# Optimization experiments

Measured on AMD Instinct MI355X. Metric: run time of the kernel, lower is better.

Reference implementation:

```python
import jax, jax.numpy as jnp
import numpy as np

DIM = 192
RC = 16
M = 64
LN_EPS = 1e-5
NORM_EPS = 1e-12


def _layernorm(x, g, b):
    mu = jnp.mean(x, axis=-1, keepdims=True)
    var = jnp.mean((x - mu) ** 2, axis=-1, keepdims=True)
    return (x - mu) / jnp.sqrt(var + LN_EPS) * g + b


def _l2norm(x):
    n = jnp.sqrt(jnp.sum(x * x, axis=-1, keepdims=True))
    return x / jnp.maximum(n, NORM_EPS)


def setup_inputs() -> dict:
    key = jax.random.key(0)
    ks = jax.random.split(key, 12)
    B, N = 8, 16384
    s_q = 1.0 / np.sqrt(DIM)
    inp = {
        "x": jax.random.normal(ks[0], (B, N, DIM), jnp.float32),
        "dict_tokens": jax.random.normal(ks[1], (B, M, DIM), jnp.float32),
        "H": 128,
        "W": 128,
        "wq_w": jax.random.normal(ks[2], (DIM, RC), jnp.float32) * s_q,
        "wq_b": jnp.zeros((RC,), jnp.float32),
        "wk_w": jax.random.normal(ks[3], (DIM, RC), jnp.float32) * s_q,
        "wk_b": jnp.zeros((RC,), jnp.float32),
        "wv_w": jax.random.normal(ks[4], (DIM, DIM), jnp.float32) * s_q,
        "wv_b": jnp.zeros((DIM,), jnp.float32),
        "qn_g": jnp.ones((RC,), jnp.float32),
        "qn_b": jnp.zeros((RC,), jnp.float32),
        "kn_g": jnp.ones((RC,), jnp.float32),
        "kn_b": jnp.zeros((RC,), jnp.float32),
        "conv_w": jax.random.normal(ks[5], (DIM, 1, 3, 3), jnp.float32) / 3.0,
        "conv_b": jnp.zeros((DIM,), jnp.float32),
        "temperature": jnp.ones((1,), jnp.float32),
    }
    return inp


def reference(x, dict_tokens, H, W, wq_w, wq_b, wk_w, wk_b, wv_w, wv_b,
              qn_g, qn_b, kn_g, kn_b, conv_w, conv_b, temperature):
    # q: (B,N,rc), k: (B,M,rc)
    q = _l2norm(_layernorm(x @ wq_w + wq_b, qn_g, qn_b))
    k = _l2norm(_layernorm(dict_tokens @ wk_w + wk_b, kn_g, kn_b))
    # cosine-similarity attention with clamped temperature
    attn = jnp.einsum("bnr,bmr->bnm", q, k) / jnp.maximum(temperature, 0.5)
    attn = jax.nn.softmax(attn, axis=-1)
    # value + depthwise-conv refinement over the M token axis (Mx1 image)
    v = dict_tokens @ wv_w + wv_b                       # (B,M,C)
    v_img = jnp.transpose(v, (0, 2, 1))[..., None]      # (B,C,M,1)
    v_img = jax.lax.conv_general_dilated(
        v_img, conv_w, window_strides=(1, 1), padding=((1, 1), (1, 1)),
        dimension_numbers=("NCHW", "OIHW", "NCHW"), feature_group_count=DIM)
    v_img = v_img + conv_b[None, :, None, None]
    v_img = jax.nn.gelu(v_img, approximate=False)
    v = jnp.transpose(v_img[..., 0], (0, 2, 1))         # (B,M,C)
    out = jnp.einsum("bnm,bmc->bnc", attn, v)           # (B,N,C)
    return out, attn
```

## Files before the change

### kernel.cpp

```cpp
#include <hip/hip_runtime.h>
#include <math.h>

#define B_   8
#define N_   16384
#define M_   64
#define C_   192
#define RC_  16

__global__ __launch_bounds__(256) void k_v_kernel(
    const float* __restrict__ dict, const float* __restrict__ wv_w,
    const float* __restrict__ wv_b, float* __restrict__ ws_v)
{
    const int idx = blockIdx.x * 256 + threadIdx.x;
    const int c   = idx % C_;
    const int row = idx / C_;
    const float* dr = dict + row * C_;
    float acc = wv_b[c];
    #pragma unroll 4
    for (int d = 0; d < C_; ++d)
        acc = fmaf(dr[d], wv_w[d * C_ + c], acc);
    ws_v[idx] = acc;
}

__global__ __launch_bounds__(256) void k_k_kernel(
    const float* __restrict__ dict, const float* __restrict__ wk_w,
    const float* __restrict__ wk_b, const float* __restrict__ kn_g,
    const float* __restrict__ kn_b, float* __restrict__ ws_k)
{
    const int b  = blockIdx.x;
    const int m  = threadIdx.x >> 2;
    const int j4 = threadIdx.x & 3;
    const int c0 = j4 * 4;
    const float* dr = dict + (b * M_ + m) * C_;

    float a0 = wk_b[c0+0], a1 = wk_b[c0+1], a2 = wk_b[c0+2], a3 = wk_b[c0+3];
    #pragma unroll 4
    for (int d4 = 0; d4 < C_/4; ++d4) {
        const float4 xv = ((const float4*)dr)[d4];
        const float4 w0 = *(const float4*)&wk_w[(d4*4+0)*RC_ + c0];
        const float4 w1 = *(const float4*)&wk_w[(d4*4+1)*RC_ + c0];
        const float4 w2 = *(const float4*)&wk_w[(d4*4+2)*RC_ + c0];
        const float4 w3 = *(const float4*)&wk_w[(d4*4+3)*RC_ + c0];
        a0 = fmaf(xv.x, w0.x, a0); a1 = fmaf(xv.x, w0.y, a1); a2 = fmaf(xv.x, w0.z, a2); a3 = fmaf(xv.x, w0.w, a3);
        a0 = fmaf(xv.y, w1.x, a0); a1 = fmaf(xv.y, w1.y, a1); a2 = fmaf(xv.y, w1.z, a2); a3 = fmaf(xv.y, w1.w, a3);
        a0 = fmaf(xv.z, w2.x, a0); a1 = fmaf(xv.z, w2.y, a1); a2 = fmaf(xv.z, w2.z, a2); a3 = fmaf(xv.z, w2.w, a3);
        a0 = fmaf(xv.w, w3.x, a0); a1 = fmaf(xv.w, w3.y, a1); a2 = fmaf(xv.w, w3.z, a2); a3 = fmaf(xv.w, w3.w, a3);
    }
    float s  = a0 + a1 + a2 + a3;
    float ss = a0*a0 + a1*a1 + a2*a2 + a3*a3;
    s  += __shfl_xor(s, 1);  s  += __shfl_xor(s, 2);
    ss += __shfl_xor(ss, 1); ss += __shfl_xor(ss, 2);
    const float mu   = s * (1.0f/16.0f);
    const float var  = ss * (1.0f/16.0f) - mu*mu;
    const float rstd = rsqrtf(var + 1e-5f);
    const float4 g4 = *(const float4*)&kn_g[c0];
    const float4 b4 = *(const float4*)&kn_b[c0];
    float y0 = (a0 - mu) * rstd * g4.x + b4.x;
    float y1 = (a1 - mu) * rstd * g4.y + b4.y;
    float y2 = (a2 - mu) * rstd * g4.z + b4.z;
    float y3 = (a3 - mu) * rstd * g4.w + b4.w;
    float n2 = y0*y0 + y1*y1 + y2*y2 + y3*y3;
    n2 += __shfl_xor(n2, 1); n2 += __shfl_xor(n2, 2);
    const float inv = 1.0f / fmaxf(sqrtf(n2), 1e-12f);
    float4 o; o.x = y0*inv; o.y = y1*inv; o.z = y2*inv; o.w = y3*inv;
    *(float4*)&ws_k[(b * M_ + m) * RC_ + c0] = o;
}

__global__ __launch_bounds__(256) void k_conv_kernel(
    const float* __restrict__ ws_v, const float* __restrict__ conv_w,
    const float* __restrict__ conv_b, float* __restrict__ ws_vg)
{
    const int idx = blockIdx.x * 256 + threadIdx.x;
    const int c   = idx % C_;
    const int m   = (idx / C_) % M_;
    const float ctr = ws_v[idx];
    const float up  = (m > 0)      ? ws_v[idx - C_] : 0.0f;
    const float dn  = (m < M_ - 1) ? ws_v[idx + C_] : 0.0f;
    const float w0 = conv_w[c*9 + 1];
    const float w1 = conv_w[c*9 + 4];
    const float w2 = conv_w[c*9 + 7];
    float t = conv_b[c];
    t = fmaf(up, w0, t); t = fmaf(ctr, w1, t); t = fmaf(dn, w2, t);
    ws_vg[idx] = 0.5f * t * (1.0f + erff(t * 0.70710678118654752f));
}

__global__ __launch_bounds__(256, 2) void k_main_kernel(
    const float* __restrict__ x, const float* __restrict__ ws_k,
    const float* __restrict__ ws_vg,
    const float* __restrict__ wq_w, const float* __restrict__ wq_b,
    const float* __restrict__ qn_g, const float* __restrict__ qn_b,
    const float* __restrict__ temp,
    float* __restrict__ out, float* __restrict__ attn_out)
{
    __shared__ float vg_s[M_ * C_];
    __shared__ float attn_s[M_ * 68];
    __shared__ float q_s[M_ * 20];
    __shared__ float k_s[M_ * RC_];

    const int tid = threadIdx.x;
    const int b   = blockIdx.x >> 8;
    const int n0  = (blockIdx.x & 255) * M_;

    {
        const float4* src = (const float4*)(ws_vg + b * (M_ * C_));
        float4*       dst = (float4*)vg_s;
        #pragma unroll
        for (int i = 0; i < 12; ++i)
            dst[tid + 256 * i] = src[tid + 256 * i];
        ((float4*)k_s)[tid] = ((const float4*)(ws_k + b * (M_ * RC_)))[tid];
    }

    const int r  = tid >> 2;
    const int j4 = tid & 3;
    const int c0 = j4 * 4;

    const float* xr = x + (size_t)(b * N_ + n0 + r) * C_;
    float a0 = wq_b[c0+0], a1 = wq_b[c0+1], a2 = wq_b[c0+2], a3 = wq_b[c0+3];
    #pragma unroll 4
    for (int d4 = 0; d4 < C_/4; ++d4) {
        const float4 xv = ((const float4*)xr)[d4];
        const float4 w0 = *(const float4*)&wq_w[(d4*4+0)*RC_ + c0];
        const float4 w1 = *(const float4*)&wq_w[(d4*4+1)*RC_ + c0];
        const float4 w2 = *(const float4*)&wq_w[(d4*4+2)*RC_ + c0];
        const float4 w3 = *(const float4*)&wq_w[(d4*4+3)*RC_ + c0];
        a0 = fmaf(xv.x, w0.x, a0); a1 = fmaf(xv.x, w0.y, a1); a2 = fmaf(xv.x, w0.z, a2); a3 = fmaf(xv.x, w0.w, a3);
        a0 = fmaf(xv.y, w1.x, a0); a1 = fmaf(xv.y, w1.y, a1); a2 = fmaf(xv.y, w1.z, a2); a3 = fmaf(xv.y, w1.w, a3);
        a0 = fmaf(xv.z, w2.x, a0); a1 = fmaf(xv.z, w2.y, a1); a2 = fmaf(xv.z, w2.z, a2); a3 = fmaf(xv.z, w2.w, a3);
        a0 = fmaf(xv.w, w3.x, a0); a1 = fmaf(xv.w, w3.y, a1); a2 = fmaf(xv.w, w3.z, a2); a3 = fmaf(xv.w, w3.w, a3);
    }
    {
        float s  = a0 + a1 + a2 + a3;
        float ss = a0*a0 + a1*a1 + a2*a2 + a3*a3;
        s  += __shfl_xor(s, 1);  s  += __shfl_xor(s, 2);
        ss += __shfl_xor(ss, 1); ss += __shfl_xor(ss, 2);
        const float mu   = s * (1.0f/16.0f);
        const float var  = ss * (1.0f/16.0f) - mu*mu;
        const float rstd = rsqrtf(var + 1e-5f);
        const float4 g4 = *(const float4*)&qn_g[c0];
        const float4 b4 = *(const float4*)&qn_b[c0];
        const float y0 = (a0 - mu) * rstd * g4.x + b4.x;
        const float y1 = (a1 - mu) * rstd * g4.y + b4.y;
        const float y2 = (a2 - mu) * rstd * g4.z + b4.z;
        const float y3 = (a3 - mu) * rstd * g4.w + b4.w;
        float n2 = y0*y0 + y1*y1 + y2*y2 + y3*y3;
        n2 += __shfl_xor(n2, 1); n2 += __shfl_xor(n2, 2);
        const float inv = 1.0f / fmaxf(sqrtf(n2), 1e-12f);
        float4 o; o.x = y0*inv; o.y = y1*inv; o.z = y2*inv; o.w = y3*inv;
        *(float4*)&q_s[r*20 + c0] = o;
    }

    __syncthreads();

    {
        const float tinv = 1.0f / fmaxf(temp[0], 0.5f);
        const float4 q0 = *(const float4*)&q_s[r*20 + 0];
        const float4 q1 = *(const float4*)&q_s[r*20 + 4];
        const float4 q2 = *(const float4*)&q_s[r*20 + 8];
        const float4 q3 = *(const float4*)&q_s[r*20 + 12];
        float sc[16];
        #pragma unroll
        for (int mm = 0; mm < 16; ++mm) {
            const int m = j4*16 + mm;
            const float4 k0 = *(const float4*)&k_s[m*RC_ + 0];
            const float4 k1 = *(const float4*)&k_s[m*RC_ + 4];
            const float4 k2 = *(const float4*)&k_s[m*RC_ + 8];
            const float4 k3 = *(const float4*)&k_s[m*RC_ + 12];
            float d = q0.x*k0.x;
            d = fmaf(q0.y, k0.y, d); d = fmaf(q0.z, k0.z, d); d = fmaf(q0.w, k0.w, d);
            d = fmaf(q1.x, k1.x, d); d = fmaf(q1.y, k1.y, d); d = fmaf(q1.z, k1.z, d); d = fmaf(q1.w, k1.w, d);
            d = fmaf(q2.x, k2.x, d); d = fmaf(q2.y, k2.y, d); d = fmaf(q2.z, k2.z, d); d = fmaf(q2.w, k2.w, d);
            d = fmaf(q3.x, k3.x, d); d = fmaf(q3.y, k3.y, d); d = fmaf(q3.z, k3.z, d); d = fmaf(q3.w, k3.w, d);
            sc[mm] = d * tinv;
        }
        float mx = sc[0];
        #pragma unroll
        for (int mm = 1; mm < 16; ++mm) mx = fmaxf(mx, sc[mm]);
        mx = fmaxf(mx, __shfl_xor(mx, 1)); mx = fmaxf(mx, __shfl_xor(mx, 2));
        float es = 0.0f;
        #pragma unroll
        for (int mm = 0; mm < 16; ++mm) { sc[mm] = expf(sc[mm] - mx); es += sc[mm]; }
        es += __shfl_xor(es, 1); es += __shfl_xor(es, 2);
        const float einv = 1.0f / es;
        float* aw = attn_out + (size_t)(b * N_ + n0 + r) * M_ + j4*16;
        #pragma unroll
        for (int mq = 0; mq < 4; ++mq) {
            float4 av;
            av.x = sc[mq*4+0]*einv; av.y = sc[mq*4+1]*einv;
            av.z = sc[mq*4+2]*einv; av.w = sc[mq*4+3]*einv;
            *(float4*)&attn_s[r*68 + j4*16 + mq*4] = av;
            ((float4*)aw)[mq] = av;
        }
    }

    __syncthreads();

    {
        float4 acc[12];
        #pragma unroll
        for (int cc = 0; cc < 12; ++cc) { acc[cc].x = 0.f; acc[cc].y = 0.f; acc[cc].z = 0.f; acc[cc].w = 0.f; }
        for (int m = 0; m < M_; ++m) {
            const float a = attn_s[r*68 + m];
            #pragma unroll
            for (int cc = 0; cc < 12; ++cc) {
                const float4 v = *(const float4*)&vg_s[m*C_ + cc*16 + c0];
                acc[cc].x = fmaf(a, v.x, acc[cc].x);
                acc[cc].y = fmaf(a, v.y, acc[cc].y);
                acc[cc].z = fmaf(a, v.z, acc[cc].z);
                acc[cc].w = fmaf(a, v.w, acc[cc].w);
            }
        }
        float* orow = out + (size_t)(b * N_ + n0 + r) * C_;
        #pragma unroll
        for (int cc = 0; cc < 12; ++cc)
            *(float4*)&orow[cc*16 + c0] = acc[cc];
    }
}

extern "C" void kernel_launch(void* const* d_in, const int* in_sizes, int n_in,
                              void* d_out, int out_size, void* d_ws, size_t ws_size,
                              hipStream_t stream) {
    const float* x      = (const float*)d_in[0];
    const float* dict   = (const float*)d_in[1];
    const float* wq_w   = (const float*)d_in[4];
    const float* wq_b   = (const float*)d_in[5];
    const float* wk_w   = (const float*)d_in[6];
    const float* wk_b   = (const float*)d_in[7];
    const float* wv_w   = (const float*)d_in[8];
    const float* wv_b   = (const float*)d_in[9];
    const float* qn_g   = (const float*)d_in[10];
    const float* qn_b   = (const float*)d_in[11];
    const float* kn_g   = (const float*)d_in[12];
    const float* kn_b   = (const float*)d_in[13];
    const float* conv_w = (const float*)d_in[14];
    const float* conv_b = (const float*)d_in[15];
    const float* temp   = (const float*)d_in[16];

    float* out  = (float*)d_out;
    float* attn = out + (size_t)B_ * N_ * C_;

    float* ws_v  = (float*)d_ws;
    float* ws_vg = ws_v  + B_ * M_ * C_;
    float* ws_k  = ws_vg + B_ * M_ * C_;

    k_v_kernel   <<<B_ * M_ * C_ / 256, 256, 0, stream>>>(dict, wv_w, wv_b, ws_v);
    k_k_kernel   <<<B_,                 256, 0, stream>>>(dict, wk_w, wk_b, kn_g, kn_b, ws_k);
    k_conv_kernel<<<B_ * M_ * C_ / 256, 256, 0, stream>>>(ws_v, conv_w, conv_b, ws_vg);
    k_main_kernel<<<B_ * (N_ / M_),     256, 0, stream>>>(x, ws_k, ws_vg, wq_w, wq_b,
                                                          qn_g, qn_b, temp, out, attn);
}
```

Measured before the change: 350.4 us.

## Read V and K from global/L1 instead of LDS, use nontemporal output stores

Removes the shared-memory staging of the per-batch gelu'd value matrix and K, so the AV product and score loop read directly from global memory through the caches. This cuts LDS from roughly 70KB to about 22KB per block, and the launch bound is raised to 4 blocks per SM to allow more occupancy. The attention and output writes become nontemporal stores to avoid polluting caches with streaming data. The trade-off is that V reads now go through the vector memory path, which has higher latency and lower bandwidth than LDS for the 64x192 reuse per block.

Result: slower. 606.5 us (+73.1%).

```diff
diff --git a/kernel.cpp b/kernel.cpp
--- a/kernel.cpp
+++ b/kernel.cpp
@@ -6,6 +6,14 @@
 #define M_   64
 #define C_   192
 #define RC_  16
+
+typedef float f32x4 __attribute__((ext_vector_type(4)));
+
+__device__ __forceinline__ void nt_store4(float* p, float a, float b, float c, float d)
+{
+    f32x4 v; v[0] = a; v[1] = b; v[2] = c; v[3] = d;
+    __builtin_nontemporal_store(v, (f32x4*)p);
+}
 
 __global__ __launch_bounds__(256) void k_v_kernel(
     const float* __restrict__ dict, const float* __restrict__ wv_w,
@@ -84,7 +92,7 @@
     ws_vg[idx] = 0.5f * t * (1.0f + erff(t * 0.70710678118654752f));
 }
 
-__global__ __launch_bounds__(256, 2) void k_main_kernel(
+__global__ __launch_bounds__(256, 4) void k_main_kernel(
     const float* __restrict__ x, const float* __restrict__ ws_k,
     const float* __restrict__ ws_vg,
     const float* __restrict__ wq_w, const float* __restrict__ wq_b,
@@ -92,23 +100,12 @@
     const float* __restrict__ temp,
     float* __restrict__ out, float* __restrict__ attn_out)
 {
-    __shared__ float vg_s[M_ * C_];
     __shared__ float attn_s[M_ * 68];
     __shared__ float q_s[M_ * 20];
-    __shared__ float k_s[M_ * RC_];
 
     const int tid = threadIdx.x;
     const int b   = blockIdx.x >> 8;
     const int n0  = (blockIdx.x & 255) * M_;
-
-    {
-        const float4* src = (const float4*)(ws_vg + b * (M_ * C_));
-        float4*       dst = (float4*)vg_s;
-        #pragma unroll
-        for (int i = 0; i < 12; ++i)
-            dst[tid + 256 * i] = src[tid + 256 * i];
-        ((float4*)k_s)[tid] = ((const float4*)(ws_k + b * (M_ * RC_)))[tid];
-    }
 
     const int r  = tid >> 2;
     const int j4 = tid & 3;
@@ -157,14 +154,15 @@
         const float4 q1 = *(const float4*)&q_s[r*20 + 4];
         const float4 q2 = *(const float4*)&q_s[r*20 + 8];
         const float4 q3 = *(const float4*)&q_s[r*20 + 12];
+        const float* kb = ws_k + b * (M_ * RC_);
         float sc[16];
         #pragma unroll
         for (int mm = 0; mm < 16; ++mm) {
             const int m = j4*16 + mm;
-            const float4 k0 = *(const float4*)&k_s[m*RC_ + 0];
-            const float4 k1 = *(const float4*)&k_s[m*RC_ + 4];
-            const float4 k2 = *(const float4*)&k_s[m*RC_ + 8];
-            const float4 k3 = *(const float4*)&k_s[m*RC_ + 12];
+            const float4 k0 = *(const float4*)&kb[m*RC_ + 0];
+            const float4 k1 = *(const float4*)&kb[m*RC_ + 4];
+            const float4 k2 = *(const float4*)&kb[m*RC_ + 8];
+            const float4 k3 = *(const float4*)&kb[m*RC_ + 12];
             float d = q0.x*k0.x;
             d = fmaf(q0.y, k0.y, d); d = fmaf(q0.z, k0.z, d); d = fmaf(q0.w, k0.w, d);
             d = fmaf(q1.x, k1.x, d); d = fmaf(q1.y, k1.y, d); d = fmaf(q1.z, k1.z, d); d = fmaf(q1.w, k1.w, d);
@@ -188,21 +186,24 @@
             av.x = sc[mq*4+0]*einv; av.y = sc[mq*4+1]*einv;
             av.z = sc[mq*4+2]*einv; av.w = sc[mq*4+3]*einv;
             *(float4*)&attn_s[r*68 + j4*16 + mq*4] = av;
-            ((float4*)aw)[mq] = av;
+            nt_store4(aw + mq*4, av.x, av.y, av.z, av.w);
         }
     }
 
     __syncthreads();
 
     {
+        const float* vgb = ws_vg + b * (M_ * C_);
         float4 acc[12];
         #pragma unroll
         for (int cc = 0; cc < 12; ++cc) { acc[cc].x = 0.f; acc[cc].y = 0.f; acc[cc].z = 0.f; acc[cc].w = 0.f; }
+        #pragma unroll 4
         for (int m = 0; m < M_; ++m) {
             const float a = attn_s[r*68 + m];
+            const float* vr = vgb + m * C_ + c0;
             #pragma unroll
             for (int cc = 0; cc < 12; ++cc) {
-                const float4 v = *(const float4*)&vg_s[m*C_ + cc*16 + c0];
+                const float4 v = *(const float4*)&vr[cc*16];
                 acc[cc].x = fmaf(a, v.x, acc[cc].x);
                 acc[cc].y = fmaf(a, v.y, acc[cc].y);
                 acc[cc].z = fmaf(a, v.z, acc[cc].z);
@@ -212,7 +213,7 @@
         float* orow = out + (size_t)(b * N_ + n0 + r) * C_;
         #pragma unroll
         for (int cc = 0; cc < 12; ++cc)
-            *(float4*)&orow[cc*16 + c0] = acc[cc];
+            nt_store4(&orow[cc*16 + c0], acc[cc].x, acc[cc].y, acc[cc].z, acc[cc].w);
     }
 }
 
```
